# Performance work log

Hardware: AMD Instinct MI355X
Metric: run time of the kernel (lower is better)

Reference implementation:

```python
import jax, jax.numpy as jnp
import numpy as np
import math

B, S, DIM, HEADS = 2, 2048, 1024, 16


def _alibi_slopes(n_heads):
    def pow2_slopes(n):
        start = 2 ** (-2 ** (-(math.log2(n) - 3)))
        return [start * start ** i for i in range(n)]
    if math.log2(n_heads).is_integer():
        slopes = pow2_slopes(n_heads)
    else:
        closest = 2 ** math.floor(math.log2(n_heads))
        slopes = pow2_slopes(closest)
        slopes += pow2_slopes(2 * closest)[0::2][: n_heads - closest]
    return np.asarray(slopes, dtype=np.float32).reshape(n_heads, 1, 1)


def setup_inputs() -> dict:
    key = jax.random.key(0)
    k1, k2, k3 = jax.random.split(key, 3)
    x = jax.random.normal(k1, (B, S, DIM), dtype=jnp.float32)
    W_qkv = jax.random.normal(k2, (3 * DIM, DIM), dtype=jnp.float32) * 0.02
    W_o = jax.random.normal(k3, (DIM, DIM), dtype=jnp.float32) * 0.02
    return {"x": x, "W_qkv": W_qkv, "W_o": W_o}


def reference(x, W_qkv, W_o):
    b, s, d = x.shape
    h = HEADS
    hd = d // h
    scale = hd ** -0.5

    qkv = x @ W_qkv.T                                   # (b, s, 3d)
    q, k, v = jnp.split(qkv, 3, axis=-1)
    q = q.reshape(b, s, h, hd).transpose(0, 2, 1, 3)    # (b, h, s, hd)
    k = k.reshape(b, s, h, hd).transpose(0, 2, 1, 3)
    v = v.reshape(b, s, h, hd).transpose(0, 2, 1, 3)

    scores = jnp.einsum('bhqd,bhkd->bhqk', q, k) * scale  # (b, h, s, s)

    pos = jnp.arange(s)
    rel = (pos[None, :] - pos[:, None]).astype(scores.dtype)  # j - i, (s, s)
    slopes = jnp.asarray(_alibi_slopes(h))                     # (h, 1, 1)
    scores = scores - slopes * rel                             # broadcast over (b,)

    causal_mask = pos[None, :] > pos[:, None]                  # True above diag
    scores = jnp.where(causal_mask, jnp.finfo(scores.dtype).min, scores)

    weights = jax.nn.softmax(scores, axis=-1)
    out = jnp.einsum('bhqk,bhkd->bhqd', weights, v)            # (b, h, s, hd)
    out = out.transpose(0, 2, 1, 3).reshape(b, s, d)
    return out @ W_o.T
```

## Files before the change

### kernel.cpp

```cpp
#include <hip/hip_runtime.h>

typedef unsigned short u16;
typedef unsigned int u32;
typedef __attribute__((ext_vector_type(8))) __bf16 bf16x8;
typedef __attribute__((ext_vector_type(4))) float f32x4;
typedef __attribute__((ext_vector_type(4))) u32 u32x4;


static __device__ __forceinline__ u16 f2bf(float f) {
  unsigned u = __builtin_bit_cast(unsigned, f);
  u += 0x7FFFu + ((u >> 16) & 1u);
  return (u16)(u >> 16);
}
static __device__ __forceinline__ float bf2f(u16 v) {
  return __builtin_bit_cast(float, (u32)v << 16);
}

static __device__ __forceinline__ void gload_lds16(const void* g, void* l) {
  __builtin_amdgcn_global_load_lds(
      (const __attribute__((address_space(1))) unsigned int*)g,
      (__attribute__((address_space(3))) unsigned int*)l, 16, 0, 0);
}

__global__ __launch_bounds__(256) void cvt_all(const float* __restrict__ x,
                                               const float* __restrict__ wq,
                                               const float* __restrict__ wo,
                                               u16* __restrict__ xb,
                                               u16* __restrict__ wqb,
                                               u16* __restrict__ wob) {
  int i = blockIdx.x * 256 + threadIdx.x;
  const float* src;
  u16* dst;
  int off;
  if (i < 1048576) {
    src = x; dst = xb; off = i;
  } else if (i < 1048576 + 786432) {
    src = wq; dst = wqb; off = i - 1048576;
  } else {
    src = wo; dst = wob; off = i - 1835008;
  }
  float4 f = ((const float4*)src)[off];
  uint2 o;
  o.x = (unsigned)f2bf(f.x) | ((unsigned)f2bf(f.y) << 16);
  o.y = (unsigned)f2bf(f.z) | ((unsigned)f2bf(f.w) << 16);
  ((uint2*)dst)[off] = o;
}

__global__ __launch_bounds__(256, 2) void gemm_qkv(
    const u16* __restrict__ A, const u16* __restrict__ Bm, int K,
    u16* __restrict__ qo, u16* __restrict__ ko, u16* __restrict__ vo) {
  __shared__ __align__(16) u16 SH[2][128 * 64];
  const int tid = threadIdx.x;
  const int lane = tid & 63, w = tid >> 6;
  const int wr = w >> 1, wc = w & 1;
  const int hfl = blockIdx.y * gridDim.x + blockIdx.x;
  const int qq = (gridDim.x * gridDim.y) >> 3;
  const int wid = (hfl & 7) * qq + (hfl >> 3);
  const int m0 = (wid % gridDim.y) * 128;
  const int n0 = (wid / gridDim.y) * 128;
  const int c16 = lane >> 4, r16 = lane & 15;

  const f32x4 zero4 = {0.f, 0.f, 0.f, 0.f};
  f32x4 acc[4][4];
#pragma unroll
  for (int r = 0; r < 4; ++r)
#pragma unroll
    for (int c = 0; c < 4; ++c) acc[r][c] = zero4;

  const int nk = K >> 6;

  auto stage = [&](int kt) {
#pragma unroll
    for (int i = 0; i < 4; ++i) {
      const int chunk = w * 4 + i;
      const int lb = chunk * 1024 + lane * 16;
      const int row = lb >> 7;
      const int rb = (lb & 127) ^ ((row & 7) << 4);
      gload_lds16(A + (size_t)(m0 + row) * K + kt * 64 + (rb >> 1),
                  (char*)&SH[0][0] + chunk * 1024);
      gload_lds16(Bm + (size_t)(n0 + row) * K + kt * 64 + (rb >> 1),
                  (char*)&SH[1][0] + chunk * 1024);
    }
  };

  stage(0);
  __syncthreads();
  for (int kt = 0; kt < nk; ++kt) {
#pragma unroll
    for (int ks = 0; ks < 2; ++ks) {
      bf16x8 af[4], bfv[4];
#pragma unroll
      for (int r = 0; r < 4; ++r) {
        const int ra = wr * 64 + r * 16 + r16;
        af[r] = *(const bf16x8*)((const char*)&SH[0][0] +
                ((ra * 128 + ks * 64 + c16 * 16) ^ ((ra & 7) << 4)));
        const int rbn = wc * 64 + r * 16 + r16;
        bfv[r] = *(const bf16x8*)((const char*)&SH[1][0] +
                ((rbn * 128 + ks * 64 + c16 * 16) ^ ((rbn & 7) << 4)));
      }
#pragma unroll
      for (int r = 0; r < 4; ++r)
#pragma unroll
        for (int c = 0; c < 4; ++c)
          acc[r][c] = __builtin_amdgcn_mfma_f32_16x16x32_bf16(
              af[r], bfv[c], acc[r][c], 0, 0, 0);
    }
    __syncthreads();
    if (kt + 1 < nk) stage(kt + 1);
    __syncthreads();
  }

  if (n0 < 2048) {
    const float qs = (n0 < 1024) ? 0.18033688f : 1.0f;
    u16* dst0 = (n0 < 1024) ? qo : ko;
#pragma unroll
    for (int r = 0; r < 4; ++r)
#pragma unroll
      for (int c = 0; c < 4; ++c)
#pragma unroll
        for (int b = 0; b < 4; ++b) {
          const int row = m0 + wr * 64 + r * 16 + 4 * c16 + b;
          const int col = n0 + wc * 64 + c * 16 + r16;
          const int hh = (col & 1023) >> 6, hd = col & 63;
          const int bi = row >> 11, s = row & 2047;
          dst0[((size_t)(bi * 16 + hh) * 2048 + s) * 64 + hd] =
              f2bf(acc[r][c][b] * qs);
        }
  } else {
#pragma unroll
    for (int r = 0; r < 4; ++r)
#pragma unroll
      for (int c = 0; c < 4; ++c)
#pragma unroll
        for (int b = 0; b < 4; b += 2) {
          const int row_l = wr * 64 + r * 16 + 4 * c16 + b;
          const int col_l = wc * 64 + c * 16 + r16;
          const u32 val = (u32)f2bf(acc[r][c][b]) |
                          ((u32)f2bf(acc[r][c][b + 1]) << 16);
          *(u32*)((char*)&SH[0][0] +
                  ((col_l * 256 + (row_l >> 1) * 4) ^ ((col_l & 7) << 4))) = val;
        }
    __syncthreads();
    const int col_l = tid >> 1, half = tid & 1;
    const int hh = (n0 - 2048 + col_l) >> 6, hd = (n0 - 2048 + col_l) & 63;
    const int bi = m0 >> 11;
    u16* dst = vo + ((size_t)(bi * 16 + hh) * 64 + hd) * 2048 +
               (m0 & 2047) + half * 64;
#pragma unroll
    for (int j = 0; j < 8; ++j) {
      const uint4 v4 = *(const uint4*)((const char*)&SH[0][0] +
          (col_l * 256 + ((half * 128 + j * 16) ^ ((col_l & 7) << 4))));
      *(uint4*)(dst + j * 8) = v4;
    }
  }
}

__global__ __launch_bounds__(128, 3) void gemm_proj(
    const u16* __restrict__ A, const u16* __restrict__ Bm, int K, int N,
    float* __restrict__ fo) {
  __shared__ __align__(16) u16 Asm[64 * 64];
  __shared__ __align__(16) u16 Bsm[128 * 64];
  const int tid = threadIdx.x;
  const int lane = tid & 63, w = tid >> 6;
  const int hfl = blockIdx.y * gridDim.x + blockIdx.x;
  const int qq = (gridDim.x * gridDim.y) >> 3;
  const int wid = (hfl & 7) * qq + (hfl >> 3);
  const int m0 = (wid % gridDim.y) * 64;
  const int n0 = (wid / gridDim.y) * 128;
  const int c16 = lane >> 4, r16 = lane & 15;

  const f32x4 zero4 = {0.f, 0.f, 0.f, 0.f};
  f32x4 acc[4][4];
#pragma unroll
  for (int r = 0; r < 4; ++r)
#pragma unroll
    for (int c = 0; c < 4; ++c) acc[r][c] = zero4;

  const int nk = K >> 6;

  auto stage = [&](int kt) {
#pragma unroll
    for (int i = 0; i < 4; ++i) {
      const int chunk = w * 4 + i;
      const int lb = chunk * 1024 + lane * 16;
      const int row = lb >> 7;
      const int rb = (lb & 127) ^ ((row & 7) << 4);
      gload_lds16(A + (size_t)(m0 + row) * K + kt * 64 + (rb >> 1),
                  (char*)&Asm[0] + chunk * 1024);
    }
#pragma unroll
    for (int i = 0; i < 8; ++i) {
      const int chunk = w * 8 + i;
      const int lb = chunk * 1024 + lane * 16;
      const int row = lb >> 7;
      const int rb = (lb & 127) ^ ((row & 7) << 4);
      gload_lds16(Bm + (size_t)(n0 + row) * K + kt * 64 + (rb >> 1),
                  (char*)&Bsm[0] + chunk * 1024);
    }
  };

  stage(0);
  __syncthreads();
  for (int kt = 0; kt < nk; ++kt) {
#pragma unroll
    for (int ks = 0; ks < 2; ++ks) {
      bf16x8 af[4], bfv[4];
#pragma unroll
      for (int r = 0; r < 4; ++r) {
        const int ra = r * 16 + r16;
        af[r] = *(const bf16x8*)((const char*)&Asm[0] +
                ((ra * 128 + ks * 64 + c16 * 16) ^ ((ra & 7) << 4)));
        const int rbn = w * 64 + r * 16 + r16;
        bfv[r] = *(const bf16x8*)((const char*)&Bsm[0] +
                ((rbn * 128 + ks * 64 + c16 * 16) ^ ((rbn & 7) << 4)));
      }
#pragma unroll
      for (int r = 0; r < 4; ++r)
#pragma unroll
        for (int c = 0; c < 4; ++c)
          acc[r][c] = __builtin_amdgcn_mfma_f32_16x16x32_bf16(
              af[r], bfv[c], acc[r][c], 0, 0, 0);
    }
    __syncthreads();
    if (kt + 1 < nk) stage(kt + 1);
    __syncthreads();
  }

#pragma unroll
  for (int r = 0; r < 4; ++r)
#pragma unroll
    for (int c = 0; c < 4; ++c)
#pragma unroll
      for (int b = 0; b < 4; ++b) {
        const int row = m0 + r * 16 + 4 * c16 + b;
        const int col = n0 + w * 64 + c * 16 + r16;
        fo[(size_t)row * N + col] = acc[r][c][b];
      }
}

__global__ __launch_bounds__(256, 5) void attn_part(const u16* __restrict__ qb,
                                                    const u16* __restrict__ kb,
                                                    const u16* __restrict__ vtb,
                                                    u16* __restrict__ ob,
                                                    u16* __restrict__ Op,
                                                    float* __restrict__ ml) {
  __shared__ __align__(16) u16 Kl[2][64 * 64];
  __shared__ __align__(16) u16 Vt[2][64 * 64];

  const int tid = threadIdx.x;
  const int lane = tid & 63, w = tid >> 6;
  const int lo = lane & 15, hi = lane >> 4;
  const int yb = blockIdx.y;
  const int h = 15 - (yb >> 1), bi = yb & 1;
  const int bh = bi * 16 + h;
  const int y = blockIdx.x;

  int qt, t0, t1, slot = 0;
  bool part;
  if (y < 16) {
    qt = 31 - y;
    const int T = qt + 1;
    t0 = T >> 1; t1 = T; part = true;
    slot = bh * 32 + (qt - 16) * 2 + 1;
  } else if (y < 32) {
    qt = 47 - y;
    const int T = qt + 1;
    t0 = 0; t1 = T >> 1; part = true;
    slot = bh * 32 + (qt - 16) * 2;
  } else {
    qt = 47 - y;
    t0 = 0; t1 = qt + 1; part = false;
  }

  const int q0 = qt * 64;
  const float slope2 = exp2f(-0.5f * (float)(h + 1)) * 1.44269504089f;
  const float s64 = slope2 * 64.f;

  const int Dt = min(32, (int)ceilf(34.f / s64));
  t1 = min(t1, Dt);

  if (part && t0 >= t1) {
#pragma unroll
    for (int g = 0; g < 4; ++g)
#pragma unroll
      for (int r = 0; r < 4; ++r) {
        const int sl = w * 16 + 4 * hi + r;
        Op[(size_t)slot * 4096 + sl * 64 + g * 16 + lo] = 0;
      }
    if (hi == 0) ml[slot * 64 + w * 16 + lo] = 0.f;
    return;
  }

  const u16* __restrict__ Q = qb + (size_t)bh * 131072;
  const u16* __restrict__ Kp = kb + (size_t)bh * 131072;
  const u16* __restrict__ Vp = vtb + (size_t)bh * 131072;

  auto stageK = [&](int t, int buf) {
#pragma unroll
    for (int i = 0; i < 2; ++i) {
      const int chunk = w * 2 + i;
      const int lb = chunk * 1024 + lane * 16;
      const int row = lb >> 7;
      const int rb = (lb & 127) ^ ((row & 7) << 4);
      gload_lds16(Kp + (size_t)(t * 64 + row) * 64 + (rb >> 1),
                  (char*)&Kl[buf][0] + chunk * 1024);
    }
  };
  auto stageV = [&](int t, int buf) {
#pragma unroll
    for (int i = 0; i < 2; ++i) {
      const int chunk = w * 2 + i;
      const int lb = chunk * 1024 + lane * 16;
      const int row = lb >> 7;
      const int rb = (lb & 127) ^ ((row & 7) << 4);
      gload_lds16(Vp + (size_t)row * 2048 + t * 64 + (rb >> 1),
                  (char*)&Vt[buf][0] + chunk * 1024);
    }
  };

  bf16x8 qf[2];
  {
    const u16* qsrc = Q + (size_t)(q0 + w * 16 + lo) * 64 + hi * 8;
    qf[0] = *(const bf16x8*)qsrc;
    qf[1] = *(const bf16x8*)(qsrc + 32);
  }

  const f32x4 zero4 = {0.f, 0.f, 0.f, 0.f};
  f32x4 oacc[4];
#pragma unroll
  for (int g = 0; g < 4; ++g) oacc[g] = zero4;
  float lsum = 0.f;

  float KC[4][4];
#pragma unroll
  for (int g = 0; g < 4; ++g)
#pragma unroll
    for (int r = 0; r < 4; ++r)
      KC[g][r] = slope2 * (float)(16 * g + 4 * hi + r);
  float ctv = 0.f;

  stageK(t0, 0);
  stageV(t0, 0);
  __syncthreads();

  for (int t = t0; t < t1; ++t) {
    const int cur = (t - t0) & 1, nxt = cur ^ 1;
    if (t + 1 < t1) {
      stageK(t + 1, nxt);
      stageV(t + 1, nxt);
    }

    f32x4 st[4];
#pragma unroll
    for (int g = 0; g < 4; ++g) {
#pragma unroll
      for (int r = 0; r < 4; ++r) st[g][r] = ctv - KC[g][r];
#pragma unroll
      for (int ks = 0; ks < 2; ++ks) {
        const int krow = g * 16 + lo;
        const bf16x8 kf = *(const bf16x8*)((const char*)&Kl[cur][0] +
            ((krow * 128 + ks * 64 + hi * 16) ^ ((krow & 7) << 4)));
        st[g] = __builtin_amdgcn_mfma_f32_16x16x32_bf16(kf, qf[ks], st[g], 0, 0, 0);
      }
    }

    if (t == qt) {
#pragma unroll
      for (int g = 0; g < 4; ++g)
#pragma unroll
        for (int r = 0; r < 4; ++r)
          if (g * 16 + 4 * hi + r > w * 16 + lo) st[g][r] = -1e30f;
    }
    float p[4][4];
    float rs = 0.f;
#pragma unroll
    for (int g = 0; g < 4; ++g)
#pragma unroll
      for (int r = 0; r < 4; ++r) {
        p[g][r] = exp2f(st[g][r]);
        rs += p[g][r];
      }
    lsum += rs;

    u32 pk[4][2];
#pragma unroll
    for (int g = 0; g < 4; ++g)
#pragma unroll
      for (int c = 0; c < 2; ++c)
        pk[g][c] = __builtin_amdgcn_perm(
            __builtin_bit_cast(u32, p[g][2 * c + 1]),
            __builtin_bit_cast(u32, p[g][2 * c]), 0x07060302u);

    bf16x8 pA[2];
#pragma unroll
    for (int u = 0; u < 2; ++u) {
      u32 x0 = pk[2 * u][0], x1 = pk[2 * u][1];
      u32 y0 = pk[2 * u + 1][0], y1 = pk[2 * u + 1][1];
      asm("v_permlane32_swap_b32 %0, %1" : "+v"(x0), "+v"(y0));
      asm("v_permlane32_swap_b32 %0, %1" : "+v"(x1), "+v"(y1));
      asm("v_permlane16_swap_b32 %0, %1" : "+v"(x0), "+v"(y0));
      asm("v_permlane16_swap_b32 %0, %1" : "+v"(x1), "+v"(y1));
      u32x4 wv;
      wv.x = x0;
      wv.y = x1;
      wv.z = y0;
      wv.w = y1;
      pA[u] = __builtin_bit_cast(bf16x8, wv);
    }

#pragma unroll
    for (int g = 0; g < 4; ++g) {
#pragma unroll
      for (int u = 0; u < 2; ++u) {
        const int vrow = g * 16 + lo;
        const bf16x8 vf = *(const bf16x8*)((const char*)&Vt[cur][0] +
            ((vrow * 128 + u * 64 + hi * 16) ^ ((vrow & 7) << 4)));
        oacc[g] = __builtin_amdgcn_mfma_f32_16x16x32_bf16(pA[u], vf, oacc[g], 0, 0, 0);
      }
    }

    ctv -= s64;
    __syncthreads();
  }

  lsum += __shfl_xor(lsum, 16, 64);
  lsum += __shfl_xor(lsum, 32, 64);
  const float inv = 1.f / lsum;
  float iv[4];
#pragma unroll
  for (int r = 0; r < 4; ++r) iv[r] = __shfl(inv, 4 * hi + r, 64);

  if (!part) {
#pragma unroll
    for (int g = 0; g < 4; ++g)
#pragma unroll
      for (int r = 0; r < 4; ++r) {
        const int s = q0 + w * 16 + 4 * hi + r;
        const int hd = g * 16 + lo;
        ob[(((size_t)bi * 2048 + s) * 16 + h) * 64 + hd] =
            f2bf(oacc[g][r] * iv[r]);
      }
  } else {
#pragma unroll
    for (int g = 0; g < 4; ++g)
#pragma unroll
      for (int r = 0; r < 4; ++r) {
        const int sl = w * 16 + 4 * hi + r;
        Op[(size_t)slot * 4096 + sl * 64 + g * 16 + lo] =
            f2bf(oacc[g][r] * iv[r]);
      }
    if (hi == 0) ml[slot * 64 + w * 16 + lo] = lsum;
  }
}

__global__ __launch_bounds__(256) void attn_comb(const u16* __restrict__ Op,
                                                 const float* __restrict__ ml,
                                                 u16* __restrict__ ob) {
  const int bh = blockIdx.x, q16 = blockIdx.y;
  const int h = bh & 15, bi = bh >> 4;
  const int qt = 16 + q16;
  const int t0c = (qt + 1) >> 1;
  const float slope2 = exp2f(-0.5f * (float)(h + 1)) * 1.44269504089f;
  const float e1 = exp2f(-slope2 * 64.f * (float)t0c);
  const int slot0 = bh * 32 + q16 * 2;
  const int row = threadIdx.x >> 2, c0 = (threadIdx.x & 3) * 16;
  const float l0 = ml[slot0 * 64 + row];
  const float l1 = ml[(slot0 + 1) * 64 + row];
  const float w0 = l0, w1 = l1 * e1;
  const float inv = 1.f / (w0 + w1);
  const float a0 = w0 * inv, a1 = w1 * inv;
  const u16* p0 = Op + (size_t)slot0 * 4096 + row * 64 + c0;
  const u16* p1 = p0 + 4096;
  u32 A0[8], A1[8];
  *(uint4*)&A0[0] = *(const uint4*)p0;
  *(uint4*)&A0[4] = *(const uint4*)(p0 + 8);
  *(uint4*)&A1[0] = *(const uint4*)p1;
  *(uint4*)&A1[4] = *(const uint4*)(p1 + 8);
  const int s = qt * 64 + row;
  u32* dst = (u32*)(ob + (((size_t)bi * 2048 + s) * 16 + h) * 64 + c0);
#pragma unroll
  for (int j = 0; j < 8; ++j) {
    const float e0 = a0 * bf2f((u16)(A0[j] & 0xffffu)) +
                     a1 * bf2f((u16)(A1[j] & 0xffffu));
    const float ee1 = a0 * bf2f((u16)(A0[j] >> 16)) +
                      a1 * bf2f((u16)(A1[j] >> 16));
    dst[j] = (u32)f2bf(e0) | ((u32)f2bf(ee1) << 16);
  }
}

extern "C" void kernel_launch(void* const* d_in, const int* in_sizes, int n_in,
                              void* d_out, int out_size, void* d_ws, size_t ws_size,
                              hipStream_t stream) {
  const float* x = (const float*)d_in[0];
  const float* Wqkv = (const float*)d_in[1];
  const float* Wo = (const float*)d_in[2];
  float* out = (float*)d_out;

  u16* xb  = (u16*)d_ws;
  u16* wqb = xb + 4194304;
  u16* wob = wqb + 3145728;
  u16* qbf = wob + 1048576;
  u16* kbf = qbf + 4194304;
  u16* vbf = kbf + 4194304;
  u16* abf = vbf + 4194304;

  u16* Op = xb;
  float* ml = (float*)wqb;

  cvt_all<<<8192, 256, 0, stream>>>(x, Wqkv, Wo, xb, wqb, wob);

  gemm_qkv<<<dim3(24, 32), 256, 0, stream>>>(xb, wqb, 1024, qbf, kbf, vbf);
  attn_part<<<dim3(48, 32), 256, 0, stream>>>(qbf, kbf, vbf, abf, Op, ml);
  attn_comb<<<dim3(32, 16), 256, 0, stream>>>(Op, ml, abf);
  gemm_proj<<<dim3(8, 64), 128, 0, stream>>>(abf, wob, 1024, 1024, out);
}
```

Before: 101.0 us.

## Drop LDS staging in attention; two waves each handle 32 query rows

The attention kernel now runs with 128 threads (2 waves), each wave processing two 16-row query groups. K and V fragments are loaded straight from global memory into registers and reused across both query groups, instead of going through double-buffered LDS with barriers. This removes the LDS traffic and the __syncthreads calls, and gives more MFMA work per loaded fragment. In exchange it relies on L1/L2 caching for K/V reuse across waves, and the extra accumulators raise register pressure.

```diff
diff --git a/kernel.cpp b/kernel.cpp
--- a/kernel.cpp
+++ b/kernel.cpp
@@ -238,15 +238,12 @@
       }
 }
 
-__global__ __launch_bounds__(256, 5) void attn_part(const u16* __restrict__ qb,
+__global__ __launch_bounds__(128, 4) void attn_part(const u16* __restrict__ qb,
                                                     const u16* __restrict__ kb,
                                                     const u16* __restrict__ vtb,
                                                     u16* __restrict__ ob,
                                                     u16* __restrict__ Op,
                                                     float* __restrict__ ml) {
-  __shared__ __align__(16) u16 Kl[2][64 * 64];
-  __shared__ __align__(16) u16 Vt[2][64 * 64];
-
   const int tid = threadIdx.x;
   const int lane = tid & 63, w = tid >> 6;
   const int lo = lane & 15, hi = lane >> 4;
@@ -281,13 +278,18 @@
 
   if (part && t0 >= t1) {
 #pragma unroll
-    for (int g = 0; g < 4; ++g)
-#pragma unroll
-      for (int r = 0; r < 4; ++r) {
-        const int sl = w * 16 + 4 * hi + r;
-        Op[(size_t)slot * 4096 + sl * 64 + g * 16 + lo] = 0;
-      }
-    if (hi == 0) ml[slot * 64 + w * 16 + lo] = 0.f;
+    for (int qg = 0; qg < 2; ++qg)
+#pragma unroll
+      for (int g = 0; g < 4; ++g)
+#pragma unroll
+        for (int r = 0; r < 4; ++r) {
+          const int sl = w * 32 + qg * 16 + 4 * hi + r;
+          Op[(size_t)slot * 4096 + sl * 64 + g * 16 + lo] = 0;
+        }
+    if (hi == 0) {
+      ml[slot * 64 + w * 32 + lo] = 0.f;
+      ml[slot * 64 + w * 32 + 16 + lo] = 0.f;
+    }
     return;
   }
 
@@ -295,41 +297,21 @@
   const u16* __restrict__ Kp = kb + (size_t)bh * 131072;
   const u16* __restrict__ Vp = vtb + (size_t)bh * 131072;
 
-  auto stageK = [&](int t, int buf) {
-#pragma unroll
-    for (int i = 0; i < 2; ++i) {
-      const int chunk = w * 2 + i;
-      const int lb = chunk * 1024 + lane * 16;
-      const int row = lb >> 7;
-      const int rb = (lb & 127) ^ ((row & 7) << 4);
-      gload_lds16(Kp + (size_t)(t * 64 + row) * 64 + (rb >> 1),
-                  (char*)&Kl[buf][0] + chunk * 1024);
-    }
-  };
-  auto stageV = [&](int t, int buf) {
-#pragma unroll
-    for (int i = 0; i < 2; ++i) {
-      const int chunk = w * 2 + i;
-      const int lb = chunk * 1024 + lane * 16;
-      const int row = lb >> 7;
-      const int rb = (lb & 127) ^ ((row & 7) << 4);
-      gload_lds16(Vp + (size_t)row * 2048 + t * 64 + (rb >> 1),
-                  (char*)&Vt[buf][0] + chunk * 1024);
-    }
-  };
-
-  bf16x8 qf[2];
-  {
-    const u16* qsrc = Q + (size_t)(q0 + w * 16 + lo) * 64 + hi * 8;
-    qf[0] = *(const bf16x8*)qsrc;
-    qf[1] = *(const bf16x8*)(qsrc + 32);
+  bf16x8 qf[2][2];
+#pragma unroll
+  for (int qg = 0; qg < 2; ++qg) {
+    const u16* qsrc = Q + (size_t)(q0 + w * 32 + qg * 16 + lo) * 64 + hi * 8;
+    qf[qg][0] = *(const bf16x8*)qsrc;
+    qf[qg][1] = *(const bf16x8*)(qsrc + 32);
   }
 
   const f32x4 zero4 = {0.f, 0.f, 0.f, 0.f};
-  f32x4 oacc[4];
-#pragma unroll
-  for (int g = 0; g < 4; ++g) oacc[g] = zero4;
-  float lsum = 0.f;
+  f32x4 oacc[2][4];
+#pragma unroll
+  for (int qg = 0; qg < 2; ++qg)
+#pragma unroll
+    for (int g = 0; g < 4; ++g) oacc[qg][g] = zero4;
+  float lsum[2] = {0.f, 0.f};
 
   float KC[4][4];
 #pragma unroll
@@ -339,117 +321,130 @@
       KC[g][r] = slope2 * (float)(16 * g + 4 * hi + r);
   float ctv = 0.f;
 
-  stageK(t0, 0);
-  stageV(t0, 0);
-  __syncthreads();
-
   for (int t = t0; t < t1; ++t) {
-    const int cur = (t - t0) & 1, nxt = cur ^ 1;
-    if (t + 1 < t1) {
-      stageK(t + 1, nxt);
-      stageV(t + 1, nxt);
-    }
-
-    f32x4 st[4];
+    f32x4 st[2][4];
 #pragma unroll
     for (int g = 0; g < 4; ++g) {
-#pragma unroll
-      for (int r = 0; r < 4; ++r) st[g][r] = ctv - KC[g][r];
-#pragma unroll
-      for (int ks = 0; ks < 2; ++ks) {
-        const int krow = g * 16 + lo;
-        const bf16x8 kf = *(const bf16x8*)((const char*)&Kl[cur][0] +
-            ((krow * 128 + ks * 64 + hi * 16) ^ ((krow & 7) << 4)));
-        st[g] = __builtin_amdgcn_mfma_f32_16x16x32_bf16(kf, qf[ks], st[g], 0, 0, 0);
+      const u16* kr = Kp + (size_t)(t * 64 + g * 16 + lo) * 64 + hi * 8;
+      const bf16x8 kf0 = *(const bf16x8*)kr;
+      const bf16x8 kf1 = *(const bf16x8*)(kr + 32);
+#pragma unroll
+      for (int qg = 0; qg < 2; ++qg) {
+#pragma unroll
+        for (int r = 0; r < 4; ++r) st[qg][g][r] = ctv - KC[g][r];
+        st[qg][g] = __builtin_amdgcn_mfma_f32_16x16x32_bf16(
+            kf0, qf[qg][0], st[qg][g], 0, 0, 0);
+        st[qg][g] = __builtin_amdgcn_mfma_f32_16x16x32_bf16(
+            kf1, qf[qg][1], st[qg][g], 0, 0, 0);
       }
     }
 
     if (t == qt) {
 #pragma unroll
+      for (int qg = 0; qg < 2; ++qg)
+#pragma unroll
+        for (int g = 0; g < 4; ++g)
+#pragma unroll
+          for (int r = 0; r < 4; ++r)
+            if (g * 16 + 4 * hi + r > w * 32 + qg * 16 + lo)
+              st[qg][g][r] = -1e30f;
+    }
+
+    bf16x8 pA[2][2];
+#pragma unroll
+    for (int qg = 0; qg < 2; ++qg) {
+      float p[4][4];
+      float rs = 0.f;
+#pragma unroll
       for (int g = 0; g < 4; ++g)
 #pragma unroll
-        for (int r = 0; r < 4; ++r)
-          if (g * 16 + 4 * hi + r > w * 16 + lo) st[g][r] = -1e30f;
-    }
-    float p[4][4];
-    float rs = 0.f;
-#pragma unroll
-    for (int g = 0; g < 4; ++g)
-#pragma unroll
-      for (int r = 0; r < 4; ++r) {
-        p[g][r] = exp2f(st[g][r]);
-        rs += p[g][r];
+        for (int r = 0; r < 4; ++r) {
+          p[g][r] = exp2f(st[qg][g][r]);
+          rs += p[g][r];
+        }
+      lsum[qg] += rs;
+
+      u32 pk[4][2];
+#pragma unroll
+      for (int g = 0; g < 4; ++g)
+#pragma unroll
+        for (int c = 0; c < 2; ++c)
+          pk[g][c] = __builtin_amdgcn_perm(
+              __builtin_bit_cast(u32, p[g][2 * c + 1]),
+              __builtin_bit_cast(u32, p[g][2 * c]), 0x07060302u);
+
+#pragma unroll
+      for (int u = 0; u < 2; ++u) {
+        u32 x0 = pk[2 * u][0], x1 = pk[2 * u][1];
+        u32 y0 = pk[2 * u + 1][0], y1 = pk[2 * u + 1][1];
+        asm("v_permlane32_swap_b32 %0, %1" : "+v"(x0), "+v"(y0));
+        asm("v_permlane32_swap_b32 %0, %1" : "+v"(x1), "+v"(y1));
+        asm("v_permlane16_swap_b32 %0, %1" : "+v"(x0), "+v"(y0));
+        asm("v_permlane16_swap_b32 %0, %1" : "+v"(x1), "+v"(y1));
+        u32x4 wv;
+        wv.x = x0;
+        wv.y = x1;
+        wv.z = y0;
+        wv.w = y1;
+        pA[qg][u] = __builtin_bit_cast(bf16x8, wv);
       }
-    lsum += rs;
-
-    u32 pk[4][2];
-#pragma unroll
-    for (int g = 0; g < 4; ++g)
-#pragma unroll
-      for (int c = 0; c < 2; ++c)
-        pk[g][c] = __builtin_amdgcn_perm(
-            __builtin_bit_cast(u32, p[g][2 * c + 1]),
-            __builtin_bit_cast(u32, p[g][2 * c]), 0x07060302u);
-
-    bf16x8 pA[2];
-#pragma unroll
-    for (int u = 0; u < 2; ++u) {
-      u32 x0 = pk[2 * u][0], x1 = pk[2 * u][1];
-      u32 y0 = pk[2 * u + 1][0], y1 = pk[2 * u + 1][1];
-      asm("v_permlane32_swap_b32 %0, %1" : "+v"(x0), "+v"(y0));
-      asm("v_permlane32_swap_b32 %0, %1" : "+v"(x1), "+v"(y1));
-      asm("v_permlane16_swap_b32 %0, %1" : "+v"(x0), "+v"(y0));
-      asm("v_permlane16_swap_b32 %0, %1" : "+v"(x1), "+v"(y1));
-      u32x4 wv;
-      wv.x = x0;
-      wv.y = x1;
-      wv.z = y0;
-      wv.w = y1;
-      pA[u] = __builtin_bit_cast(bf16x8, wv);
     }
 
 #pragma unroll
     for (int g = 0; g < 4; ++g) {
 #pragma unroll
       for (int u = 0; u < 2; ++u) {
-        const int vrow = g * 16 + lo;
-        const bf16x8 vf = *(const bf16x8*)((const char*)&Vt[cur][0] +
-            ((vrow * 128 + u * 64 + hi * 16) ^ ((vrow & 7) << 4)));
-        oacc[g] = __builtin_amdgcn_mfma_f32_16x16x32_bf16(pA[u], vf, oacc[g], 0, 0, 0);
+        const bf16x8 vf = *(const bf16x8*)(Vp +
+            (size_t)(g * 16 + lo) * 2048 + t * 64 + u * 32 + hi * 8);
+#pragma unroll
+        for (int qg = 0; qg < 2; ++qg)
+          oacc[qg][g] = __builtin_amdgcn_mfma_f32_16x16x32_bf16(
+              pA[qg][u], vf, oacc[qg][g], 0, 0, 0);
       }
     }
 
     ctv -= s64;
-    __syncthreads();
-  }
-
-  lsum += __shfl_xor(lsum, 16, 64);
-  lsum += __shfl_xor(lsum, 32, 64);
-  const float inv = 1.f / lsum;
-  float iv[4];
-#pragma unroll
-  for (int r = 0; r < 4; ++r) iv[r] = __shfl(inv, 4 * hi + r, 64);
+  }
+
+  float iv[2][4];
+#pragma unroll
+  for (int qg = 0; qg < 2; ++qg) {
+    float ls = lsum[qg];
+    ls += __shfl_xor(ls, 16, 64);
+    ls += __shfl_xor(ls, 32, 64);
+    const float inv = 1.f / ls;
+#pragma unroll
+    for (int r = 0; r < 4; ++r) iv[qg][r] = __shfl(inv, 4 * hi + r, 64);
+    lsum[qg] = ls;
+  }
 
   if (!part) {
 #pragma unroll
-    for (int g = 0; g < 4; ++g)
-#pragma unroll
-      for (int r = 0; r < 4; ++r) {
-        const int s = q0 + w * 16 + 4 * hi + r;
-        const int hd = g * 16 + lo;
-        ob[(((size_t)bi * 2048 + s) * 16 + h) * 64 + hd] =
-            f2bf(oacc[g][r] * iv[r]);
-      }
+    for (int qg = 0; qg < 2; ++qg)
+#pragma unroll
+      for (int g = 0; g < 4; ++g)
+#pragma unroll
+        for (int r = 0; r < 4; ++r) {
+          const int s = q0 + w * 32 + qg * 16 + 4 * hi + r;
+          const int hd = g * 16 + lo;
+          ob[(((size_t)bi * 2048 + s) * 16 + h) * 64 + hd] =
+              f2bf(oacc[qg][g][r] * iv[qg][r]);
+        }
   } else {
 #pragma unroll
-    for (int g = 0; g < 4; ++g)
-#pragma unroll
-      for (int r = 0; r < 4; ++r) {
-        const int sl = w * 16 + 4 * hi + r;
-        Op[(size_t)slot * 4096 + sl * 64 + g * 16 + lo] =
-            f2bf(oacc[g][r] * iv[r]);
-      }
-    if (hi == 0) ml[slot * 64 + w * 16 + lo] = lsum;
+    for (int qg = 0; qg < 2; ++qg)
+#pragma unroll
+      for (int g = 0; g < 4; ++g)
+#pragma unroll
+        for (int r = 0; r < 4; ++r) {
+          const int sl = w * 32 + qg * 16 + 4 * hi + r;
+          Op[(size_t)slot * 4096 + sl * 64 + g * 16 + lo] =
+              f2bf(oacc[qg][g][r] * iv[qg][r]);
+        }
+    if (hi == 0) {
+      ml[slot * 64 + w * 32 + lo] = lsum[0];
+      ml[slot * 64 + w * 32 + 16 + lo] = lsum[1];
+    }
   }
 }
 
@@ -510,7 +505,7 @@
   cvt_all<<<8192, 256, 0, stream>>>(x, Wqkv, Wo, xb, wqb, wob);
 
   gemm_qkv<<<dim3(24, 32), 256, 0, stream>>>(xb, wqb, 1024, qbf, kbf, vbf);
-  attn_part<<<dim3(48, 32), 256, 0, stream>>>(qbf, kbf, vbf, abf, Op, ml);
+  attn_part<<<dim3(48, 32), 128, 0, stream>>>(qbf, kbf, vbf, abf, Op, ml);
   attn_comb<<<dim3(32, 16), 256, 0, stream>>>(Op, ml, abf);
   gemm_proj<<<dim3(8, 64), 128, 0, stream>>>(abf, wob, 1024, 1024, out);
 }
```

After: 141.5 us. +40.1%, slower.
